# Kernel optimization log

Measured on AMD Instinct MI355X. Metric: run time of the kernel, lower is better.

## Reference

```python
import jax, jax.numpy as jnp
import numpy as np

B, S, E = 2, 2048, 2048
H, D = 16, 128  # num_heads, head_dim = E // H


def setup_inputs() -> dict:
    key = jax.random.key(0)
    ks = jax.random.split(key, 5)
    hidden_states = jax.random.normal(ks[0], (B, S, E), dtype=jnp.float32) * 0.02
    wq = jax.random.normal(ks[1], (E, E), dtype=jnp.float32) * 0.02
    wk = jax.random.normal(ks[2], (E, E), dtype=jnp.float32) * 0.02
    wv = jax.random.normal(ks[3], (E, E), dtype=jnp.float32) * 0.02
    wo = jax.random.normal(ks[4], (E, E), dtype=jnp.float32) * 0.02
    bo = jnp.zeros((E,), dtype=jnp.float32)
    return {"hidden_states": hidden_states, "wq": wq, "wk": wk, "wv": wv, "wo": wo, "bo": bo}


def _split_heads(x):
    # [B, S, E] -> [B, H, S, D]
    return x.reshape(B, S, H, D).transpose(0, 2, 1, 3)


def reference(hidden_states, wq, wk, wv, wo, bo):
    q = _split_heads(hidden_states @ wq)  # [B,H,S,D]
    k = _split_heads(hidden_states @ wk)
    v = _split_heads(hidden_states @ wv)

    # GPT-Neo: no 1/sqrt(d) scaling; scores computed in fp32
    attn_weights = jnp.einsum("bhqd,bhkd->bhqk", q.astype(jnp.float32), k.astype(jnp.float32))

    causal_mask = jnp.tril(jnp.ones((S, S), dtype=bool))  # bias[:, :, :S, :S]
    # Faithful quirk: masked positions get the GLOBAL MIN of attn_weights, not -inf
    mask_value = jnp.min(attn_weights)
    attn_weights = jnp.where(causal_mask, attn_weights, mask_value)

    attn_weights = jax.nn.softmax(attn_weights, axis=-1).astype(v.dtype)
    attn_output = jnp.einsum("bhqk,bhkd->bhqd", attn_weights, v)  # [B,H,S,D]

    # merge heads: [B,H,S,D] -> [B,S,E]
    attn_output = attn_output.transpose(0, 2, 1, 3).reshape(B, S, E)
    attn_output = attn_output @ wo + bo
    return attn_output
```

## Files before the change

kernel.cpp:

```cpp
#include <hip/hip_runtime.h>

typedef unsigned short u16;
typedef unsigned int   u32;
typedef __attribute__((ext_vector_type(4))) float f32x4;
typedef __attribute__((ext_vector_type(4))) u32   u32x4;
typedef __attribute__((ext_vector_type(8))) __bf16 bf16x8;

#define S_LEN 2048
#define EMB   2048
#define NH    16
#define HD    128
#define NBH   32
#define MTOT  4096
#define NBMIN 512

__device__ __forceinline__ u16 f2bf(float f) {
    u32 u = __float_as_uint(f);
    return (u16)((u + 0x7FFFu + ((u >> 16) & 1u)) >> 16);
}
__device__ __forceinline__ float bf2f(u16 v) {
    return __uint_as_float(((u32)v) << 16);
}
__device__ __forceinline__ bf16x8 ld_frag(const u16* p) {
    return __builtin_bit_cast(bf16x8, *(const u32x4*)p);
}
__device__ __forceinline__ void gld_lds16(const void* g, void* l) {
    __builtin_amdgcn_global_load_lds(
        (__attribute__((address_space(1))) void*)(g),
        (__attribute__((address_space(3))) void*)(l), 16, 0, 0);
}

__global__ __launch_bounds__(256) void cast_x_kernel(
    const float* __restrict__ X, u16* __restrict__ Xb)
{
    const size_t i = ((size_t)blockIdx.x * 256 + threadIdx.x) * 8;
    float4 a = *(const float4*)&X[i];
    float4 b = *(const float4*)&X[i + 4];
    u32x4 o;
    o.x = (u32)f2bf(a.x) | ((u32)f2bf(a.y) << 16);
    o.y = (u32)f2bf(a.z) | ((u32)f2bf(a.w) << 16);
    o.z = (u32)f2bf(b.x) | ((u32)f2bf(b.y) << 16);
    o.w = (u32)f2bf(b.z) | ((u32)f2bf(b.w) << 16);
    *(u32x4*)&Xb[i] = o;
}

__global__ __launch_bounds__(256) void transpose_cast_w_kernel(
    const float* __restrict__ W0, const float* __restrict__ W1,
    const float* __restrict__ W2, const float* __restrict__ W3,
    u16* __restrict__ T0, u16* __restrict__ T1,
    u16* __restrict__ T2, u16* __restrict__ T3)
{
    __shared__ float Ls[64][68];
    const int t = threadIdx.x;
    const int n0 = blockIdx.x * 64, k0 = blockIdx.y * 64;
    const int z = blockIdx.z;
    const float* __restrict__ W = (z == 0) ? W0 : (z == 1) ? W1 : (z == 2) ? W2 : W3;
    u16* __restrict__ T = (z == 0) ? T0 : (z == 1) ? T1 : (z == 2) ? T2 : T3;

#pragma unroll
    for (int p = 0; p < 4; ++p) {
        const int r = (t >> 4) + 16 * p;
        const int c = (t & 15) * 4;
        *(float4*)&Ls[r][c] = *(const float4*)&W[(size_t)(k0 + r) * EMB + n0 + c];
    }
    __syncthreads();
    const int nl = t >> 2, q = t & 3;
    u32 pk[8];
#pragma unroll
    for (int j = 0; j < 8; ++j) {
        u16 lo = f2bf(Ls[q * 16 + 2 * j][nl]);
        u16 hi = f2bf(Ls[q * 16 + 2 * j + 1][nl]);
        pk[j] = (u32)lo | ((u32)hi << 16);
    }
    u32x4 o0 = {pk[0], pk[1], pk[2], pk[3]};
    u32x4 o1 = {pk[4], pk[5], pk[6], pk[7]};
    u16* dst = &T[(size_t)(n0 + nl) * EMB + k0 + q * 16];
    *(u32x4*)&dst[0] = o0;
    *(u32x4*)&dst[8] = o1;
}

__global__ __launch_bounds__(256) void transpose_v_kernel(
    const u16* __restrict__ V, u16* __restrict__ Vt)
{
    __shared__ u16 Ls[64][72];
    const int t = threadIdx.x;
    const int s0 = blockIdx.x * 64, d0 = blockIdx.y * 64, bh = blockIdx.z;
    const u16* __restrict__ src0 = V + ((size_t)bh * S_LEN) * HD;
    {
        const int r = t >> 2, c0 = (t & 3) * 16;
        const u16* src = &src0[(size_t)(s0 + r) * HD + d0 + c0];
        *(u32x4*)&Ls[r][c0]     = *(const u32x4*)&src[0];
        *(u32x4*)&Ls[r][c0 + 8] = *(const u32x4*)&src[8];
    }
    __syncthreads();
    const int dl = t >> 2, q = t & 3;
    u32 pk[8];
#pragma unroll
    for (int j = 0; j < 8; ++j) {
        u16 lo = Ls[q * 16 + 2 * j][dl];
        u16 hi = Ls[q * 16 + 2 * j + 1][dl];
        pk[j] = (u32)lo | ((u32)hi << 16);
    }
    u32x4 o0 = {pk[0], pk[1], pk[2], pk[3]};
    u32x4 o1 = {pk[4], pk[5], pk[6], pk[7]};
    u16* dst = &Vt[((size_t)bh * HD + d0 + dl) * S_LEN + s0 + q * 16];
    *(u32x4*)&dst[0] = o0;
    *(u32x4*)&dst[8] = o1;
}

__global__ __launch_bounds__(256) void gemm_qkv_mfma(
    const u16* __restrict__ Xb,
    const u16* __restrict__ Wtq, const u16* __restrict__ Wtk,
    const u16* __restrict__ Wtv,
    u16* __restrict__ Qo, u16* __restrict__ Ko, u16* __restrict__ Vo)
{
    __shared__ __attribute__((aligned(16))) u16 As[128 * 32];
    __shared__ __attribute__((aligned(16))) u16 Bs[128 * 32];
    const int t = threadIdx.x;
    const int w = t >> 6, lane = t & 63;
    const int wy = w >> 1, wx = w & 1;
    const int n0 = blockIdx.x * 128, m0 = blockIdx.y * 128;
    const int z = blockIdx.z;
    const u16* __restrict__ Wt = (z == 0) ? Wtq : (z == 1) ? Wtk : Wtv;
    u16* __restrict__ O = (z == 0) ? Qo : (z == 1) ? Ko : Vo;

    const int srow = lane >> 2, scol = (lane & 3) * 8;
    const u16* Ag = &Xb[(size_t)(m0 + w * 32 + srow) * EMB + scol];
    const u16* Bg = &Wt[(size_t)(n0 + w * 32 + srow) * EMB + scol];
    u16* Al0 = &As[(w * 32) * 32];
    u16* Al1 = &As[(w * 32 + 16) * 32];
    u16* Bl0 = &Bs[(w * 32) * 32];
    u16* Bl1 = &Bs[(w * 32 + 16) * 32];

    const int fm = lane & 15, fk = (lane >> 4) * 8;
    f32x4 acc[4][4];
#pragma unroll
    for (int i = 0; i < 4; ++i)
#pragma unroll
        for (int j = 0; j < 4; ++j) acc[i][j] = (f32x4)0.0f;

    for (int k0 = 0; k0 < EMB; k0 += 32) {
        __syncthreads();
        gld_lds16(Ag + k0, Al0);
        gld_lds16(Ag + 16 * EMB + k0, Al1);
        gld_lds16(Bg + k0, Bl0);
        gld_lds16(Bg + 16 * EMB + k0, Bl1);
        __syncthreads();
        bf16x8 af[4], bfr[4];
#pragma unroll
        for (int mi = 0; mi < 4; ++mi)
            af[mi] = ld_frag(&As[(64 * wy + 16 * mi + fm) * 32 + fk]);
#pragma unroll
        for (int ni = 0; ni < 4; ++ni)
            bfr[ni] = ld_frag(&Bs[(64 * wx + 16 * ni + fm) * 32 + fk]);
#pragma unroll
        for (int mi = 0; mi < 4; ++mi)
#pragma unroll
            for (int ni = 0; ni < 4; ++ni)
                acc[mi][ni] = __builtin_amdgcn_mfma_f32_16x16x32_bf16(
                    af[mi], bfr[ni], acc[mi][ni], 0, 0, 0);
    }

    const int q4 = (lane >> 4) * 4;
#pragma unroll
    for (int mi = 0; mi < 4; ++mi)
#pragma unroll
        for (int ni = 0; ni < 4; ++ni) {
            const int n = n0 + 64 * wx + 16 * ni + (lane & 15);
            const int h = n >> 7, d = n & 127;
#pragma unroll
            for (int r = 0; r < 4; ++r) {
                const int m = m0 + 64 * wy + 16 * mi + q4 + r;
                const int bb = m >> 11, s = m & 2047;
                O[(((size_t)(bb * NH + h) * S_LEN) + s) * HD + d] = f2bf(acc[mi][ni][r]);
            }
        }
}

__global__ __launch_bounds__(256) void gemm_out_mfma(
    const u16* __restrict__ Ab, const u16* __restrict__ Wto,
    const float* __restrict__ bias, float* __restrict__ Out)
{
    __shared__ __attribute__((aligned(16))) u16 As[128 * 32];
    __shared__ __attribute__((aligned(16))) u16 Bs[128 * 32];
    const int t = threadIdx.x;
    const int w = t >> 6, lane = t & 63;
    const int wy = w >> 1, wx = w & 1;
    const int n0 = blockIdx.x * 128, m0 = blockIdx.y * 128;

    const int srow = lane >> 2, scol = (lane & 3) * 8;
    const u16* Ag = &Ab[(size_t)(m0 + w * 32 + srow) * EMB + scol];
    const u16* Bg = &Wto[(size_t)(n0 + w * 32 + srow) * EMB + scol];
    u16* Al0 = &As[(w * 32) * 32];
    u16* Al1 = &As[(w * 32 + 16) * 32];
    u16* Bl0 = &Bs[(w * 32) * 32];
    u16* Bl1 = &Bs[(w * 32 + 16) * 32];

    const int fm = lane & 15, fk = (lane >> 4) * 8;
    f32x4 acc[4][4];
#pragma unroll
    for (int i = 0; i < 4; ++i)
#pragma unroll
        for (int j = 0; j < 4; ++j) acc[i][j] = (f32x4)0.0f;

    for (int k0 = 0; k0 < EMB; k0 += 32) {
        __syncthreads();
        gld_lds16(Ag + k0, Al0);
        gld_lds16(Ag + 16 * EMB + k0, Al1);
        gld_lds16(Bg + k0, Bl0);
        gld_lds16(Bg + 16 * EMB + k0, Bl1);
        __syncthreads();
        bf16x8 af[4], bfr[4];
#pragma unroll
        for (int mi = 0; mi < 4; ++mi)
            af[mi] = ld_frag(&As[(64 * wy + 16 * mi + fm) * 32 + fk]);
#pragma unroll
        for (int ni = 0; ni < 4; ++ni)
            bfr[ni] = ld_frag(&Bs[(64 * wx + 16 * ni + fm) * 32 + fk]);
#pragma unroll
        for (int mi = 0; mi < 4; ++mi)
#pragma unroll
            for (int ni = 0; ni < 4; ++ni)
                acc[mi][ni] = __builtin_amdgcn_mfma_f32_16x16x32_bf16(
                    af[mi], bfr[ni], acc[mi][ni], 0, 0, 0);
    }

    const int q4 = (lane >> 4) * 4;
#pragma unroll
    for (int mi = 0; mi < 4; ++mi)
#pragma unroll
        for (int ni = 0; ni < 4; ++ni) {
            const int n = n0 + 64 * wx + 16 * ni + (lane & 15);
            const float bv = bias[n];
#pragma unroll
            for (int r = 0; r < 4; ++r) {
                const int m = m0 + 64 * wy + 16 * mi + q4 + r;
                Out[(size_t)m * EMB + n] = acc[mi][ni][r] + bv;
            }
        }
}

__global__ __launch_bounds__(256) void reduce_min_kernel(
    const float* __restrict__ bm, float* __restrict__ minval)
{
    __shared__ float sm[256];
    const int t = threadIdx.x;
    float m = 3.0e38f;
    for (int i = t; i < NBMIN; i += 256) m = fminf(m, bm[i]);
    sm[t] = m;
    __syncthreads();
    for (int sft = 128; sft > 0; sft >>= 1) {
        if (t < sft) sm[t] = fminf(sm[t], sm[t + sft]);
        __syncthreads();
    }
    if (t == 0) minval[0] = sm[0];
}

__global__ __launch_bounds__(128) void vchunk_sum_kernel(
    const u16* __restrict__ V, float* __restrict__ csum)
{
    const int chunk = blockIdx.x, bh = blockIdx.y, d = threadIdx.x;
    const u16* vb = V + ((size_t)bh * S_LEN + chunk * 64) * HD + d;
    float s = 0.0f;
    for (int r = 0; r < 64; ++r) s += bf2f(vb[(size_t)r * HD]);
    csum[((size_t)bh * 32 + chunk) * HD + d] = s;
}

__global__ __launch_bounds__(128) void vchunk_suffix_kernel(
    const float* __restrict__ csum, float* __restrict__ csuf)
{
    const int bh = blockIdx.x, d = threadIdx.x;
    float run = 0.0f;
    for (int c = 31; c >= 0; --c) {
        const size_t idx = ((size_t)bh * 32 + c) * HD + d;
        csuf[idx] = run;
        run += csum[idx];
    }
}

__global__ __launch_bounds__(128) void vsuffix_kernel(
    const u16* __restrict__ V, const float* __restrict__ csuf,
    u16* __restrict__ vsuf)
{
    const int chunk = blockIdx.x, bh = blockIdx.y, d = threadIdx.x;
    float run = csuf[((size_t)bh * 32 + chunk) * HD + d];
    const size_t base = ((size_t)bh * S_LEN + chunk * 64) * HD + d;
    for (int r = 63; r >= 0; --r) {
        vsuf[base + (size_t)r * HD] = f2bf(run);
        run += bf2f(V[base + (size_t)r * HD]);
    }
}

__global__ __launch_bounds__(256) void attn_mfma(
    const u16* __restrict__ Q, const u16* __restrict__ K,
    const u16* __restrict__ Vt,
    u16* __restrict__ pacc0, u16* __restrict__ pacc1,
    float* __restrict__ den_p, float* __restrict__ blockmin)
{
    __shared__ __attribute__((aligned(16))) u16 Ps[128 * 136];
    __shared__ __attribute__((aligned(16))) u16 Cs[3 * 128 * 32];
    __shared__ float den_l[2][128];
    __shared__ float smn[256];

    const int t = threadIdx.x;
    const int w = t >> 6, lane = t & 63;
    const int wy = w >> 1, wx = w & 1;

    const int d_id = blockIdx.y * 16 + blockIdx.x;
    const int f_log = (d_id & 7) * 64 + (d_id >> 3);
    const int pp = (f_log & 15) >> 1, hpar = f_log & 1;
    const int bh = f_log >> 4;
    const int b = bh >> 4, h = bh & 15;

    const u16* __restrict__ Kg  = K + (size_t)bh * S_LEN * HD;
    const u16* __restrict__ Vtg = Vt + (size_t)bh * HD * S_LEN;
    u16* __restrict__ pacc = hpar ? pacc1 : pacc0;

    const int srow = lane >> 2;
    const int scol = ((lane & 3) ^ ((lane >> 3) & 3)) * 8;
    const int fm = lane & 15, fk = (lane >> 4) * 8;
    const int fkc = ((lane >> 4) ^ ((fm >> 1) & 3)) * 8;
    const int q4 = (lane >> 4) * 4;
    const int wrow = w * 32;
    u16* const cs_w = Cs + wrow * 32;

#define CSB(c_) (cs_w + (c_) * 4096)
#define STAGE_K(c_, j0_, dd_) do { \
        const u16* g_ = &Kg[(size_t)((j0_) + wrow + srow) * HD + (dd_) * 32 + scol]; \
        gld_lds16(g_, CSB(c_)); \
        gld_lds16(g_ + 16 * HD, CSB(c_) + 512); } while (0)
#define STAGE_V(c_, j0_, ss_) do { \
        const u16* g_ = &Vtg[(size_t)(wrow + srow) * S_LEN + (j0_) + (ss_) * 32 + scol]; \
        gld_lds16(g_, CSB(c_)); \
        gld_lds16(g_ + 16 * S_LEN, CSB(c_) + 512); } while (0)
#define WAITBAR2() do { \
        asm volatile("s_waitcnt lgkmcnt(0)" ::: "memory"); \
        asm volatile("s_waitcnt vmcnt(2)" ::: "memory"); \
        __builtin_amdgcn_s_barrier(); \
        __builtin_amdgcn_sched_barrier(0); } while (0)

    float mn = 3.0e38f;
    int cur = 0;

    STAGE_K(0, hpar * 128, 0);
    STAGE_K(1, hpar * 128, 1);
    asm volatile("s_waitcnt vmcnt(2)" ::: "memory");
    __builtin_amdgcn_s_barrier();
    __builtin_amdgcn_sched_barrier(0);

    for (int pass = 0; pass < 2; ++pass) {
        const int qt = pass ? (15 - pp) : pp;
        const int i0 = qt * 128;
        const u16* __restrict__ Qg = Q + ((size_t)bh * S_LEN + i0) * HD;

        bf16x8 af[4][4];
#pragma unroll
        for (int mi = 0; mi < 4; ++mi)
#pragma unroll
            for (int dk = 0; dk < 4; ++dk)
                af[mi][dk] = ld_frag(
                    &Qg[(size_t)(64 * wy + 16 * mi + fm) * HD + dk * 32 + fk]);

        f32x4 oacc[4][4];
#pragma unroll
        for (int i = 0; i < 4; ++i)
#pragma unroll
            for (int j = 0; j < 4; ++j) oacc[i][j] = (f32x4)0.0f;
        float den[4][4] = {};

        for (int ji = 0; ji < 8; ++ji) {
            const int jt = hpar + 2 * ji;
            const int j0 = jt * 128;
            const bool causal = (jt <= qt);
            const bool hn = (ji < 7) || (pass == 0);
            const int nj0 = (ji < 7) ? (jt + 2) * 128 : hpar * 128;

            f32x4 sacc[4][4];
#pragma unroll
            for (int i = 0; i < 4; ++i)
#pragma unroll
                for (int j = 0; j < 4; ++j) sacc[i][j] = (f32x4)0.0f;

#pragma unroll
            for (int dk = 0; dk < 4; ++dk) {
                int c2 = cur - 1; if (c2 < 0) c2 += 3;
                if (dk == 0)      STAGE_K(c2, j0, 2);
                else if (dk == 1) STAGE_K(c2, j0, 3);
                else if (dk == 2) {
                    if (causal)  STAGE_V(c2, j0, 0);
                    else if (hn) STAGE_K(c2, nj0, 0);
                    else         STAGE_K(c2, 0, 0);
                } else {
                    if (causal)  STAGE_V(c2, j0, 1);
                    else if (hn) STAGE_K(c2, nj0, 1);
                    else         STAGE_K(c2, 0, 0);
                }
                bf16x8 bfr[4];
#pragma unroll
                for (int ni = 0; ni < 4; ++ni)
                    bfr[ni] = ld_frag(Cs + cur * 4096
                                      + (64 * wx + 16 * ni + fm) * 32 + fkc);
                __builtin_amdgcn_s_setprio(1);
#pragma unroll
                for (int mi = 0; mi < 4; ++mi)
#pragma unroll
                    for (int ni = 0; ni < 4; ++ni)
                        sacc[mi][ni] = __builtin_amdgcn_mfma_f32_16x16x32_bf16(
                            af[mi][dk], bfr[ni], sacc[mi][ni], 0, 0, 0);
                __builtin_amdgcn_s_setprio(0);

                if (dk == 3) {
                    if (causal) {
                        const bool dg = (jt == qt);
#pragma unroll
                        for (int mi = 0; mi < 4; ++mi) {
                            const int rbase = 64 * wy + 16 * mi + q4;
#pragma unroll
                            for (int ni = 0; ni < 4; ++ni) {
                                const int cl = 64 * wx + 16 * ni + fm;
                                const int jg = j0 + cl;
#pragma unroll
                                for (int r = 0; r < 4; ++r) {
                                    const float s = sacc[mi][ni][r];
                                    mn = fminf(mn, s);
                                    float e = __expf(s);
                                    if (dg && jg > i0 + rbase + r) e = 0.0f;
                                    den[mi][r] += e;
                                    Ps[(rbase + r) * 136 + cl] = f2bf(e);
                                }
                            }
                        }
                    } else {
#pragma unroll
                        for (int mi = 0; mi < 4; ++mi)
#pragma unroll
                            for (int ni = 0; ni < 4; ++ni)
#pragma unroll
                                for (int r = 0; r < 4; ++r)
                                    mn = fminf(mn, sacc[mi][ni][r]);
                    }
                }
                WAITBAR2();
                cur = (cur == 2) ? 0 : cur + 1;
            }

            if (causal) {
#pragma unroll
                for (int sk = 0; sk < 4; ++sk) {
                    int c2 = cur - 1; if (c2 < 0) c2 += 3;
                    if (sk == 0)      STAGE_V(c2, j0, 2);
                    else if (sk == 1) STAGE_V(c2, j0, 3);
                    else if (sk == 2) {
                        if (hn) STAGE_K(c2, nj0, 0); else STAGE_K(c2, 0, 0);
                    } else {
                        if (hn) STAGE_K(c2, nj0, 1); else STAGE_K(c2, 0, 0);
                    }
                    bf16x8 pa[4], pb[4];
#pragma unroll
                    for (int mi = 0; mi < 4; ++mi)
                        pa[mi] = ld_frag(&Ps[(64 * wy + 16 * mi + fm) * 136
                                             + sk * 32 + fk]);
#pragma unroll
                    for (int ni = 0; ni < 4; ++ni)
                        pb[ni] = ld_frag(Cs + cur * 4096
                                         + (64 * wx + 16 * ni + fm) * 32 + fkc);
                    __builtin_amdgcn_s_setprio(1);
#pragma unroll
                    for (int mi = 0; mi < 4; ++mi)
#pragma unroll
                        for (int ni = 0; ni < 4; ++ni)
                            oacc[mi][ni] = __builtin_amdgcn_mfma_f32_16x16x32_bf16(
                                pa[mi], pb[ni], oacc[mi][ni], 0, 0, 0);
                    __builtin_amdgcn_s_setprio(0);
                    WAITBAR2();
                    cur = (cur == 2) ? 0 : cur + 1;
                }
            }
        }

#pragma unroll
        for (int mi = 0; mi < 4; ++mi)
#pragma unroll
            for (int r = 0; r < 4; ++r) {
                float v = den[mi][r];
                v += __shfl_xor(v, 1, 64);
                v += __shfl_xor(v, 2, 64);
                v += __shfl_xor(v, 4, 64);
                v += __shfl_xor(v, 8, 64);
                den[mi][r] = v;
            }
        __syncthreads();
        if ((lane & 15) == 0) {
#pragma unroll
            for (int mi = 0; mi < 4; ++mi)
#pragma unroll
                for (int r = 0; r < 4; ++r)
                    den_l[wx][64 * wy + 16 * mi + q4 + r] = den[mi][r];
        }
        __syncthreads();
        if (t < 128)
            den_p[((size_t)hpar * NBH + bh) * S_LEN + i0 + t] =
                den_l[0][t] + den_l[1][t];

#pragma unroll
        for (int mi = 0; mi < 4; ++mi)
#pragma unroll
            for (int ni = 0; ni < 4; ++ni) {
                const int d = 64 * wx + 16 * ni + fm;
#pragma unroll
                for (int r = 0; r < 4; ++r) {
                    const int row = 64 * wy + 16 * mi + q4 + r;
                    pacc[((size_t)b * S_LEN + i0 + row) * EMB + h * HD + d] =
                        f2bf(oacc[mi][ni][r]);
                }
            }
        __syncthreads();
    }

    smn[t] = mn;
    __syncthreads();
    for (int sft = 128; sft > 0; sft >>= 1) {
        if (t < sft) smn[t] = fminf(smn[t], smn[t + sft]);
        __syncthreads();
    }
    if (t == 0) blockmin[d_id] = smn[0];

#undef CSB
#undef STAGE_K
#undef STAGE_V
#undef WAITBAR2
}

__global__ __launch_bounds__(256) void finalize_kernel(
    u16* __restrict__ outm, const u16* __restrict__ pacc1,
    const u16* __restrict__ vsuf, const float* __restrict__ den_p,
    const float* __restrict__ minval)
{
    const size_t i = ((size_t)blockIdx.x * 256 + threadIdx.x) * 8;
    const int e = (int)(i & (EMB - 1));
    const int m = (int)(i / EMB);
    const int b = m >> 11, s = m & 2047;
    const int hh = e >> 7, d = e & 127;
    const int bh = b * NH + hh;
    const float em = __expf(minval[0]);
    const float den = den_p[(size_t)bh * S_LEN + s]
                    + den_p[((size_t)NBH + bh) * S_LEN + s]
                    + (float)(S_LEN - 1 - s) * em;
    const float inv = 1.0f / den;
    u32x4 a = *(const u32x4*)&outm[i];
    u32x4 cc = *(const u32x4*)&pacc1[i];
    u32x4 vv = *(const u32x4*)&vsuf[((size_t)bh * S_LEN + s) * HD + d];
    const u16* pa = (const u16*)&a;
    const u16* pc = (const u16*)&cc;
    const u16* pv = (const u16*)&vv;
    u16 ov[8];
#pragma unroll
    for (int j = 0; j < 8; ++j) {
        const float v = bf2f(pa[j]) + bf2f(pc[j]) + em * bf2f(pv[j]);
        ov[j] = f2bf(v * inv);
    }
    *(u32x4*)&outm[i] = *(const u32x4*)ov;
}

extern "C" void kernel_launch(void* const* d_in, const int* in_sizes, int n_in,
                              void* d_out, int out_size, void* d_ws, size_t ws_size,
                              hipStream_t stream)
{
    (void)in_sizes; (void)n_in; (void)out_size; (void)ws_size;
    const float* hs = (const float*)d_in[0];
    const float* wq = (const float*)d_in[1];
    const float* wk = (const float*)d_in[2];
    const float* wv = (const float*)d_in[3];
    const float* wo = (const float*)d_in[4];
    const float* bo = (const float*)d_in[5];
    float* out = (float*)d_out;

    char* p = (char*)d_ws;
    const size_t TS = (size_t)NBH * S_LEN * HD;
    u16* Xb   = (u16*)p; p += (size_t)MTOT * EMB * 2;
    u16* Wtq  = (u16*)p; p += (size_t)EMB * EMB * 2;
    u16* Wtk  = (u16*)p; p += (size_t)EMB * EMB * 2;
    u16* Wtv  = (u16*)p; p += (size_t)EMB * EMB * 2;
    u16* Wto  = (u16*)p; p += (size_t)EMB * EMB * 2;
    u16* Qb   = (u16*)p; p += TS * 2;
    u16* Kb   = (u16*)p; p += TS * 2;
    u16* Vb   = (u16*)p; p += TS * 2;
    u16* Vtb  = (u16*)p; p += TS * 2;
    u16* outm = (u16*)p; p += (size_t)MTOT * EMB * 2;
    u16* vsuf = (u16*)p; p += TS * 2;
    float* csum     = (float*)p; p += (size_t)NBH * 32 * HD * 4;
    float* csuf     = (float*)p; p += (size_t)NBH * 32 * HD * 4;
    float* blockmin = (float*)p; p += 1024 * 4;
    float* minval   = (float*)p; p += 64;
    float* den_p    = (float*)p; p += (size_t)2 * NBH * S_LEN * 4;
    u16* pacc1 = Xb;

    cast_x_kernel<<<4096, 256, 0, stream>>>(hs, Xb);
    transpose_cast_w_kernel<<<dim3(32, 32, 4), 256, 0, stream>>>(
        wq, wk, wv, wo, Wtq, Wtk, Wtv, Wto);

    gemm_qkv_mfma<<<dim3(EMB / 128, MTOT / 128, 3), 256, 0, stream>>>(
        Xb, Wtq, Wtk, Wtv, Qb, Kb, Vb);

    transpose_v_kernel<<<dim3(32, 2, NBH), 256, 0, stream>>>(Vb, Vtb);
    vchunk_sum_kernel<<<dim3(32, NBH), 128, 0, stream>>>(Vb, csum);
    vchunk_suffix_kernel<<<NBH, 128, 0, stream>>>(csum, csuf);
    vsuffix_kernel<<<dim3(32, NBH), 128, 0, stream>>>(Vb, csuf, vsuf);

    attn_mfma<<<dim3(16, NBH), 256, 0, stream>>>(
        Qb, Kb, Vtb, outm, pacc1, den_p, blockmin);

    reduce_min_kernel<<<1, 256, 0, stream>>>(blockmin, minval);

    finalize_kernel<<<(MTOT * EMB / 8) / 256, 256, 0, stream>>>(
        outm, pacc1, vsuf, den_p, minval);

    gemm_out_mfma<<<dim3(EMB / 128, MTOT / 128), 256, 0, stream>>>(
        outm, Wto, bo, out);
}
```

Baseline: 463.2 us.

## Load K/V fragments directly from global memory, dropping LDS triple-buffer pipeline

Removes the triple-buffered global-to-LDS staging of K and V tiles and their per-step barriers. K and V MFMA fragments are now loaded straight from global memory into registers, and launch bounds request two blocks per CU. This cuts LDS use and barrier traffic so occupancy can rise. In exchange it loses the software prefetch overlap and the swizzled shared reuse across waves, so each wave refetches K/V fragments from cache with exposed latency.

```diff
diff --git a/kernel.cpp b/kernel.cpp
--- a/kernel.cpp
+++ b/kernel.cpp
@@ -291,14 +291,13 @@
     }
 }
 
-__global__ __launch_bounds__(256) void attn_mfma(
+__global__ __launch_bounds__(256, 2) void attn_mfma(
     const u16* __restrict__ Q, const u16* __restrict__ K,
     const u16* __restrict__ Vt,
     u16* __restrict__ pacc0, u16* __restrict__ pacc1,
     float* __restrict__ den_p, float* __restrict__ blockmin)
 {
     __shared__ __attribute__((aligned(16))) u16 Ps[128 * 136];
-    __shared__ __attribute__((aligned(16))) u16 Cs[3 * 128 * 32];
     __shared__ float den_l[2][128];
     __shared__ float smn[256];
 
@@ -316,37 +315,10 @@
     const u16* __restrict__ Vtg = Vt + (size_t)bh * HD * S_LEN;
     u16* __restrict__ pacc = hpar ? pacc1 : pacc0;
 
-    const int srow = lane >> 2;
-    const int scol = ((lane & 3) ^ ((lane >> 3) & 3)) * 8;
     const int fm = lane & 15, fk = (lane >> 4) * 8;
-    const int fkc = ((lane >> 4) ^ ((fm >> 1) & 3)) * 8;
     const int q4 = (lane >> 4) * 4;
-    const int wrow = w * 32;
-    u16* const cs_w = Cs + wrow * 32;
-
-#define CSB(c_) (cs_w + (c_) * 4096)
-#define STAGE_K(c_, j0_, dd_) do { \
-        const u16* g_ = &Kg[(size_t)((j0_) + wrow + srow) * HD + (dd_) * 32 + scol]; \
-        gld_lds16(g_, CSB(c_)); \
-        gld_lds16(g_ + 16 * HD, CSB(c_) + 512); } while (0)
-#define STAGE_V(c_, j0_, ss_) do { \
-        const u16* g_ = &Vtg[(size_t)(wrow + srow) * S_LEN + (j0_) + (ss_) * 32 + scol]; \
-        gld_lds16(g_, CSB(c_)); \
-        gld_lds16(g_ + 16 * S_LEN, CSB(c_) + 512); } while (0)
-#define WAITBAR2() do { \
-        asm volatile("s_waitcnt lgkmcnt(0)" ::: "memory"); \
-        asm volatile("s_waitcnt vmcnt(2)" ::: "memory"); \
-        __builtin_amdgcn_s_barrier(); \
-        __builtin_amdgcn_sched_barrier(0); } while (0)
 
     float mn = 3.0e38f;
-    int cur = 0;
-
-    STAGE_K(0, hpar * 128, 0);
-    STAGE_K(1, hpar * 128, 1);
-    asm volatile("s_waitcnt vmcnt(2)" ::: "memory");
-    __builtin_amdgcn_s_barrier();
-    __builtin_amdgcn_sched_barrier(0);
 
     for (int pass = 0; pass < 2; ++pass) {
         const int qt = pass ? (15 - pp) : pp;
@@ -372,8 +344,6 @@
             const int jt = hpar + 2 * ji;
             const int j0 = jt * 128;
             const bool causal = (jt <= qt);
-            const bool hn = (ji < 7) || (pass == 0);
-            const int nj0 = (ji < 7) ? (jt + 2) * 128 : hpar * 128;
 
             f32x4 sacc[4][4];
 #pragma unroll
@@ -383,23 +353,12 @@
 
 #pragma unroll
             for (int dk = 0; dk < 4; ++dk) {
-                int c2 = cur - 1; if (c2 < 0) c2 += 3;
-                if (dk == 0)      STAGE_K(c2, j0, 2);
-                else if (dk == 1) STAGE_K(c2, j0, 3);
-                else if (dk == 2) {
-                    if (causal)  STAGE_V(c2, j0, 0);
-                    else if (hn) STAGE_K(c2, nj0, 0);
-                    else         STAGE_K(c2, 0, 0);
-                } else {
-                    if (causal)  STAGE_V(c2, j0, 1);
-                    else if (hn) STAGE_K(c2, nj0, 1);
-                    else         STAGE_K(c2, 0, 0);
-                }
                 bf16x8 bfr[4];
 #pragma unroll
                 for (int ni = 0; ni < 4; ++ni)
-                    bfr[ni] = ld_frag(Cs + cur * 4096
-                                      + (64 * wx + 16 * ni + fm) * 32 + fkc);
+                    bfr[ni] = ld_frag(
+                        &Kg[(size_t)(j0 + 64 * wx + 16 * ni + fm) * HD
+                            + dk * 32 + fk]);
                 __builtin_amdgcn_s_setprio(1);
 #pragma unroll
                 for (int mi = 0; mi < 4; ++mi)
@@ -408,62 +367,43 @@
                         sacc[mi][ni] = __builtin_amdgcn_mfma_f32_16x16x32_bf16(
                             af[mi][dk], bfr[ni], sacc[mi][ni], 0, 0, 0);
                 __builtin_amdgcn_s_setprio(0);
-
-                if (dk == 3) {
-                    if (causal) {
-                        const bool dg = (jt == qt);
-#pragma unroll
-                        for (int mi = 0; mi < 4; ++mi) {
-                            const int rbase = 64 * wy + 16 * mi + q4;
-#pragma unroll
-                            for (int ni = 0; ni < 4; ++ni) {
-                                const int cl = 64 * wx + 16 * ni + fm;
-                                const int jg = j0 + cl;
-#pragma unroll
-                                for (int r = 0; r < 4; ++r) {
-                                    const float s = sacc[mi][ni][r];
-                                    mn = fminf(mn, s);
-                                    float e = __expf(s);
-                                    if (dg && jg > i0 + rbase + r) e = 0.0f;
-                                    den[mi][r] += e;
-                                    Ps[(rbase + r) * 136 + cl] = f2bf(e);
-                                }
-                            }
+            }
+
+            if (causal) {
+                const bool dg = (jt == qt);
+#pragma unroll
+                for (int mi = 0; mi < 4; ++mi) {
+                    const int rbase = 64 * wy + 16 * mi + q4;
+#pragma unroll
+                    for (int ni = 0; ni < 4; ++ni) {
+                        const int cl = 64 * wx + 16 * ni + fm;
+                        const int jg = j0 + cl;
+#pragma unroll
+                        for (int r = 0; r < 4; ++r) {
+                            const float s = sacc[mi][ni][r];
+                            mn = fminf(mn, s);
+                            float e = __expf(s);
+                            if (dg && jg > i0 + rbase + r) e = 0.0f;
+                            den[mi][r] += e;
+                            Ps[(rbase + r) * 136 + cl] = f2bf(e);
                         }
-                    } else {
-#pragma unroll
-                        for (int mi = 0; mi < 4; ++mi)
-#pragma unroll
-                            for (int ni = 0; ni < 4; ++ni)
-#pragma unroll
-                                for (int r = 0; r < 4; ++r)
-                                    mn = fminf(mn, sacc[mi][ni][r]);
                     }
                 }
-                WAITBAR2();
-                cur = (cur == 2) ? 0 : cur + 1;
-            }
-
-            if (causal) {
+                asm volatile("s_waitcnt lgkmcnt(0)" ::: "memory");
+                __builtin_amdgcn_s_barrier();
+
 #pragma unroll
                 for (int sk = 0; sk < 4; ++sk) {
-                    int c2 = cur - 1; if (c2 < 0) c2 += 3;
-                    if (sk == 0)      STAGE_V(c2, j0, 2);
-                    else if (sk == 1) STAGE_V(c2, j0, 3);
-                    else if (sk == 2) {
-                        if (hn) STAGE_K(c2, nj0, 0); else STAGE_K(c2, 0, 0);
-                    } else {
-                        if (hn) STAGE_K(c2, nj0, 1); else STAGE_K(c2, 0, 0);
-                    }
                     bf16x8 pa[4], pb[4];
+#pragma unroll
+                    for (int ni = 0; ni < 4; ++ni)
+                        pb[ni] = ld_frag(
+                            &Vtg[(size_t)(64 * wx + 16 * ni + fm) * S_LEN
+                                 + j0 + sk * 32 + fk]);
 #pragma unroll
                     for (int mi = 0; mi < 4; ++mi)
                         pa[mi] = ld_frag(&Ps[(64 * wy + 16 * mi + fm) * 136
                                              + sk * 32 + fk]);
-#pragma unroll
-                    for (int ni = 0; ni < 4; ++ni)
-                        pb[ni] = ld_frag(Cs + cur * 4096
-                                         + (64 * wx + 16 * ni + fm) * 32 + fkc);
                     __builtin_amdgcn_s_setprio(1);
 #pragma unroll
                     for (int mi = 0; mi < 4; ++mi)
@@ -472,9 +412,16 @@
                             oacc[mi][ni] = __builtin_amdgcn_mfma_f32_16x16x32_bf16(
                                 pa[mi], pb[ni], oacc[mi][ni], 0, 0, 0);
                     __builtin_amdgcn_s_setprio(0);
-                    WAITBAR2();
-                    cur = (cur == 2) ? 0 : cur + 1;
                 }
+                __builtin_amdgcn_s_barrier();
+            } else {
+#pragma unroll
+                for (int mi = 0; mi < 4; ++mi)
+#pragma unroll
+                    for (int ni = 0; ni < 4; ++ni)
+#pragma unroll
+                        for (int r = 0; r < 4; ++r)
+                            mn = fminf(mn, sacc[mi][ni][r]);
             }
         }
 
@@ -524,11 +471,6 @@
         __syncthreads();
     }
     if (t == 0) blockmin[d_id] = smn[0];
-
-#undef CSB
-#undef STAGE_K
-#undef STAGE_V
-#undef WAITBAR2
 }
 
 __global__ __launch_bounds__(256) void finalize_kernel(
```

Measured after the change: 747.6 us. 61.4% more time.
